# Kernel tuning notes

Measured on AMD Instinct MI355X. Metric: run time of the kernel, lower is better.

Reference implementation:

```python
import jax, jax.numpy as jnp
import numpy as np

HID = 2048
NH = 16
HD = HID // NH  # 128
SEQ = 2048
BSZ = 2
NEG = -1e9


def setup_inputs() -> dict:
    key = jax.random.key(0)
    ks = jax.random.split(key, 9)
    s = 0.02
    hidden_states = jax.random.normal(ks[0], (BSZ, SEQ, HID), jnp.float32)
    # additive causal mask [1,1,S,S]
    causal = jnp.tril(jnp.ones((SEQ, SEQ), jnp.bool_))
    attention_mask = jnp.where(causal, 0.0, NEG).astype(jnp.float32)[None, None]
    Wq = jax.random.normal(ks[1], (HID, NH * HD), jnp.float32) * s
    bq = jax.random.normal(ks[2], (NH * HD,), jnp.float32) * s
    Wk = jax.random.normal(ks[3], (HID, NH * HD), jnp.float32) * s
    bk = jax.random.normal(ks[4], (NH * HD,), jnp.float32) * s
    Wv = jax.random.normal(ks[5], (HID, NH * HD), jnp.float32) * s
    bv = jax.random.normal(ks[6], (NH * HD,), jnp.float32) * s
    Wo = jax.random.normal(ks[7], (NH * HD, HID), jnp.float32) * s
    return {"hidden_states": hidden_states, "attention_mask": attention_mask,
            "Wq": Wq, "bq": bq, "Wk": Wk, "bk": bk, "Wv": Wv, "bv": bv, "Wo": Wo}


def reference(hidden_states, attention_mask, Wq, bq, Wk, bk, Wv, bv, Wo):
    b, s, _ = hidden_states.shape
    # projections -> [b, h, s, d]
    q = (hidden_states @ Wq + bq).reshape(b, s, NH, HD).transpose(0, 2, 1, 3)
    k = (hidden_states @ Wk + bk).reshape(b, s, NH, HD).transpose(0, 2, 1, 3)
    v = (hidden_states @ Wv + bv).reshape(b, s, NH, HD).transpose(0, 2, 1, 3)
    # eager attention, materializing [b,h,s,s] scores as in the original
    scores = jnp.einsum('bhqd,bhkd->bhqk', q, k) / jnp.sqrt(jnp.float32(HD))
    scores = scores + attention_mask
    probs = jax.nn.softmax(scores.astype(jnp.float32), axis=-1).astype(q.dtype)
    ctx = jnp.einsum('bhqk,bhkd->bhqd', probs, v)
    ctx = ctx.transpose(0, 2, 1, 3).reshape(b, s, NH * HD)
    return ctx @ Wo
```

## Files before the change

### kernel.cpp

```cpp
#include <hip/hip_runtime.h>

#define SEQ 2048
#define HIDDEN 2048
#define NHEAD 16
#define HDIM 128
#define BSZ 2

typedef __attribute__((ext_vector_type(8))) short bf16x8;
typedef __attribute__((ext_vector_type(4))) float f32x4;
typedef __attribute__((ext_vector_type(16))) float f32x16;
typedef unsigned short u16;
typedef unsigned int u32;

__device__ __forceinline__ u16 f2bf(float f) {
  union { float f; u32 u; } v; v.f = f;
  u32 r = v.u + 0x7FFF + ((v.u >> 16) & 1);
  return (u16)(r >> 16);
}

__device__ __forceinline__ void gload_lds16(const void* g, void* l) {
  __builtin_amdgcn_global_load_lds((const __attribute__((address_space(1))) u32*)g,
                                   (__attribute__((address_space(3))) u32*)l, 16, 0, 0);
}

__device__ __forceinline__ u32 pkbf(float lo, float hi_) {
  u32 r;
  asm("v_cvt_pk_bf16_f32 %0, %1, %2" : "=v"(r) : "v"(lo), "v"(hi_));
  return r;
}

__device__ __forceinline__ void pl32swap(u32& a, u32& b) {
  asm("v_permlane32_swap_b32 %0, %1" : "+v"(a), "+v"(b));
}

__global__ void conv_hs_kernel(const float4* __restrict__ in, uint4* __restrict__ out) {
  int i = blockIdx.x * 256 + threadIdx.x;
  float4 a = in[2 * i], b = in[2 * i + 1];
  uint4 o;
  o.x = (u32)f2bf(a.x) | ((u32)f2bf(a.y) << 16);
  o.y = (u32)f2bf(a.z) | ((u32)f2bf(a.w) << 16);
  o.z = (u32)f2bf(b.x) | ((u32)f2bf(b.y) << 16);
  o.w = (u32)f2bf(b.z) | ((u32)f2bf(b.w) << 16);
  out[i] = o;
}

__global__ void transw_kernel(const float* __restrict__ W0, const float* __restrict__ W1,
                              const float* __restrict__ W2, const float* __restrict__ W3,
                              u16* __restrict__ T0, u16* __restrict__ T1,
                              u16* __restrict__ T2, u16* __restrict__ T3) {
  __shared__ float tile[32][33];
  const float* W; u16* T;
  switch (blockIdx.z) {
    case 0: W = W0; T = T0; break;
    case 1: W = W1; T = T1; break;
    case 2: W = W2; T = T2; break;
    default: W = W3; T = T3; break;
  }
  int n0 = blockIdx.x * 32, k0 = blockIdx.y * 32;
  int tx = threadIdx.x, ty = threadIdx.y;
  #pragma unroll
  for (int r = ty; r < 32; r += 8) tile[r][tx] = W[(k0 + r) * HIDDEN + n0 + tx];
  __syncthreads();
  #pragma unroll
  for (int r = ty; r < 32; r += 8) T[(n0 + r) * HIDDEN + k0 + tx] = f2bf(tile[tx][r]);
}

__global__ __launch_bounds__(256, 2)
void qkv_gemm(const u16* __restrict__ hsb,
              const u16* __restrict__ wqT, const u16* __restrict__ wkT, const u16* __restrict__ wvT,
              const float* __restrict__ bq, const float* __restrict__ bk, const float* __restrict__ bv,
              u16* __restrict__ Qb, u16* __restrict__ Kb, u16* __restrict__ Vb) {
  __shared__ u16 As[128 * 32];
  __shared__ u16 Bs[128 * 32];
  const int z = blockIdx.z;
  const u16* Bt = (z == 0) ? wqT : (z == 1) ? wkT : wvT;
  const float* bias = (z == 0) ? bq : (z == 1) ? bk : bv;
  u16* dst = (z == 0) ? Qb : (z == 1) ? Kb : Vb;
  const float scale = (z == 0) ? 0.08838834764831845f * 1.4426950408889634f : 1.0f;
  const int m0 = blockIdx.y * 128, n0 = blockIdx.x * 128;
  const int tid = threadIdx.x, lane = tid & 63, w = tid >> 6;
  const int wr = w >> 1, wc = w & 1, l15 = lane & 15, l4 = lane >> 4;

  f32x4 acc[4][4] = {};
  for (int k0 = 0; k0 < HIDDEN; k0 += 32) {
    __syncthreads();
    #pragma unroll
    for (int i = 0; i < 2; i++) {
      int c = tid + i * 256;
      gload_lds16(hsb + (m0 + (c >> 2)) * HIDDEN + k0 + (c & 3) * 8, &As[c * 8]);
    }
    #pragma unroll
    for (int i = 0; i < 2; i++) {
      int c = tid + i * 256;
      gload_lds16(Bt + (n0 + (c >> 2)) * HIDDEN + k0 + (c & 3) * 8, &Bs[c * 8]);
    }
    __syncthreads();
    bf16x8 a[4], b[4];
    #pragma unroll
    for (int mi = 0; mi < 4; mi++)
      a[mi] = *(const bf16x8*)&As[(wr * 64 + mi * 16 + l15) * 32 + l4 * 8];
    #pragma unroll
    for (int ni = 0; ni < 4; ni++)
      b[ni] = *(const bf16x8*)&Bs[(wc * 64 + ni * 16 + l15) * 32 + l4 * 8];
    #pragma unroll
    for (int mi = 0; mi < 4; mi++)
      #pragma unroll
      for (int ni = 0; ni < 4; ni++)
        acc[mi][ni] = __builtin_amdgcn_mfma_f32_16x16x32_bf16(a[mi], b[ni], acc[mi][ni], 0, 0, 0);
  }
  #pragma unroll
  for (int mi = 0; mi < 4; mi++) {
    #pragma unroll
    for (int ni = 0; ni < 4; ni++) {
      int n = n0 + wc * 64 + ni * 16 + l15;
      float bv_ = bias[n];
      int h_ = n >> 7, d_ = n & 127;
      #pragma unroll
      for (int r = 0; r < 4; r++) {
        int m = m0 + wr * 64 + mi * 16 + l4 * 4 + r;
        int b_ = m >> 11, s_ = m & 2047;
        dst[(((b_ * NHEAD + h_) * SEQ) + s_) * HDIM + d_] = f2bf((acc[mi][ni][r] + bv_) * scale);
      }
    }
  }
}

__global__ void transv_kernel(const u16* __restrict__ V, u16* __restrict__ VT) {
  __shared__ u16 tile[32][33];
  int bh = blockIdx.z;
  int d0 = blockIdx.x * 32, s0 = blockIdx.y * 32;
  const u16* Vp = V + (size_t)bh * SEQ * HDIM;
  u16* Tp = VT + (size_t)bh * HDIM * SEQ;
  int tx = threadIdx.x, ty = threadIdx.y;
  #pragma unroll
  for (int r = ty; r < 32; r += 8) tile[r][tx] = Vp[(s0 + r) * HDIM + d0 + tx];
  __syncthreads();
  #pragma unroll
  for (int r = ty; r < 32; r += 8) Tp[(d0 + r) * SEQ + s0 + tx] = tile[tx][r];
}

__device__ __forceinline__ void stage_tiles(u16* KLb, u16* VLb,
                                            const u16* Kg0, const u16* Vg0,
                                            int j, int w, int lane) {
  const u16* Kg = Kg0 + j * (64 * HDIM);
  const u16* Vg = Vg0 + j * 64;
  #pragma unroll
  for (int i = 0; i < 4; i++) {
    const int c = (w * 4 + i) * 64 + lane;
    const int row = c >> 4;
    const int inb = ((c & 15) * 16) ^ ((row & 7) << 4);
    gload_lds16(Kg + row * HDIM + (inb >> 1), (char*)KLb + c * 16);
  }
  #pragma unroll
  for (int i = 0; i < 4; i++) {
    const int c = (w * 4 + i) * 64 + lane;
    const int row = c >> 3;
    const int inb = ((c & 7) * 16) ^ ((row & 7) << 4);
    gload_lds16(Vg + row * SEQ + (inb >> 1), (char*)VLb + c * 16);
  }
}

__global__ __launch_bounds__(256)
void attn_kernel(const u16* __restrict__ Qb, const u16* __restrict__ Kb,
                 const u16* __restrict__ VbT, u16* __restrict__ ctx) {
  __shared__ u16 KL[2][64 * 128];
  __shared__ u16 VL[2][128 * 64];

  const int n = blockIdx.x;
  const int xcd = n & 7, slot = n >> 3;
  const int bh = xcd * 4 + (slot >> 3);
  const int xp = slot & 7;
  const int b = bh >> 4, h = bh & 15;
  const int tid = threadIdx.x, lane = tid & 63, w = tid >> 6;
  const int l31 = lane & 31, hi = lane >> 5;

  const u16* Kg0 = Kb + (size_t)bh * SEQ * HDIM;
  const u16* Vg0 = VbT + (size_t)bh * HDIM * SEQ;
  const u16* Qg0 = Qb + (size_t)bh * SEQ * HDIM;

  for (int ph = 0; ph < 2; ph++) {
    const int qt = ph ? (15 - xp) : xp;
    const int NT = 2 * qt + 2;
    const int q0w = qt * 128 + w * 32;
    const int qlane = q0w + l31;

    bf16x8 qf[8];
    #pragma unroll
    for (int c = 0; c < 8; c++)
      qf[c] = *(const bf16x8*)(Qg0 + (size_t)qlane * HDIM + c * 16 + hi * 8);

    f32x16 o0 = {}, o1 = {}, o2 = {}, o3 = {};
    float m_run = -1e30f, l_run = 0.0f;

    int cb = 0;
    stage_tiles(&KL[0][0], &VL[0][0], Kg0, Vg0, 0, w, lane);
    __syncthreads();

    for (int j = 0; j < NT; j++) {
      if (j + 1 < NT)
        stage_tiles(&KL[cb ^ 1][0], &VL[cb ^ 1][0], Kg0, Vg0, j + 1, w, lane);

      f32x16 s0 = {}, s1 = {};
      #pragma unroll
      for (int c = 0; c < 8; c++) {
        const int cbyte = c * 32 + hi * 16;
        const int r0 = l31, r1 = 32 + l31;
        bf16x8 k0 = *(const bf16x8*)((const char*)&KL[cb][0] + (r0 * 256 + (cbyte ^ ((r0 & 7) << 4))));
        bf16x8 k1 = *(const bf16x8*)((const char*)&KL[cb][0] + (r1 * 256 + (cbyte ^ ((r1 & 7) << 4))));
        s0 = __builtin_amdgcn_mfma_f32_32x32x16_bf16(k0, qf[c], s0, 0, 0, 0);
        s1 = __builtin_amdgcn_mfma_f32_32x32x16_bf16(k1, qf[c], s1, 0, 0, 0);
      }

      if (j >= NT - 2) {
        const int kvb = j * 64 + 4 * hi;
        #pragma unroll
        for (int r = 0; r < 16; r++) {
          const int kr = kvb + (r & 3) + 8 * (r >> 2);
          if (kr > qlane) s0[r] = -1e9f;
          if (kr + 32 > qlane) s1[r] = -1e9f;
        }
      }

      float pm = s0[0];
      #pragma unroll
      for (int r = 1; r < 16; r++) pm = fmaxf(pm, s0[r]);
      #pragma unroll
      for (int r = 0; r < 16; r++) pm = fmaxf(pm, s1[r]);
      pm = fmaxf(pm, __shfl_xor(pm, 32));

      if (!__all(pm - m_run <= 8.0f)) {
        const float mn = fmaxf(m_run, pm);
        const float al = exp2f(m_run - mn);
        l_run *= al;
        #pragma unroll
        for (int r = 0; r < 16; r++) {
          const float ar = __shfl(al, (r & 3) + 8 * (r >> 2) + 4 * hi);
          o0[r] *= ar; o1[r] *= ar; o2[r] *= ar; o3[r] *= ar;
        }
        m_run = mn;
      }

      float rs = 0.0f;
      #pragma unroll
      for (int r = 0; r < 16; r++) { s0[r] = exp2f(s0[r] - m_run); rs += s0[r]; }
      #pragma unroll
      for (int r = 0; r < 16; r++) { s1[r] = exp2f(s1[r] - m_run); rs += s1[r]; }
      rs += __shfl_xor(rs, 32);
      l_run += rs;

      union { u32 wd[4]; bf16x8 v; } pa0, pa1, pa2, pa3;
      { u32 A0 = pkbf(s0[0], s0[1]),  B0 = pkbf(s0[4], s0[5]);  pl32swap(A0, B0);
        u32 A1 = pkbf(s0[2], s0[3]),  B1 = pkbf(s0[6], s0[7]);  pl32swap(A1, B1);
        pa0.wd[0] = A0; pa0.wd[1] = A1; pa0.wd[2] = B0; pa0.wd[3] = B1; }
      { u32 A0 = pkbf(s0[8], s0[9]),  B0 = pkbf(s0[12], s0[13]); pl32swap(A0, B0);
        u32 A1 = pkbf(s0[10], s0[11]), B1 = pkbf(s0[14], s0[15]); pl32swap(A1, B1);
        pa1.wd[0] = A0; pa1.wd[1] = A1; pa1.wd[2] = B0; pa1.wd[3] = B1; }
      { u32 A0 = pkbf(s1[0], s1[1]),  B0 = pkbf(s1[4], s1[5]);  pl32swap(A0, B0);
        u32 A1 = pkbf(s1[2], s1[3]),  B1 = pkbf(s1[6], s1[7]);  pl32swap(A1, B1);
        pa2.wd[0] = A0; pa2.wd[1] = A1; pa2.wd[2] = B0; pa2.wd[3] = B1; }
      { u32 A0 = pkbf(s1[8], s1[9]),  B0 = pkbf(s1[12], s1[13]); pl32swap(A0, B0);
        u32 A1 = pkbf(s1[10], s1[11]), B1 = pkbf(s1[14], s1[15]); pl32swap(A1, B1);
        pa3.wd[0] = A0; pa3.wd[1] = A1; pa3.wd[2] = B0; pa3.wd[3] = B1; }

#define PV_D(OD, DS) { \
      const int row = (DS) * 32 + l31; \
      const int sw = (row & 7) << 4; \
      const char* vbase = (const char*)&VL[cb][0] + row * 128; \
      bf16x8 v0 = *(const bf16x8*)(vbase + ((  0 + hi * 16) ^ sw)); \
      bf16x8 v1 = *(const bf16x8*)(vbase + (( 32 + hi * 16) ^ sw)); \
      bf16x8 v2 = *(const bf16x8*)(vbase + (( 64 + hi * 16) ^ sw)); \
      bf16x8 v3 = *(const bf16x8*)(vbase + (( 96 + hi * 16) ^ sw)); \
      OD = __builtin_amdgcn_mfma_f32_32x32x16_bf16(pa0.v, v0, OD, 0, 0, 0); \
      OD = __builtin_amdgcn_mfma_f32_32x32x16_bf16(pa1.v, v1, OD, 0, 0, 0); \
      OD = __builtin_amdgcn_mfma_f32_32x32x16_bf16(pa2.v, v2, OD, 0, 0, 0); \
      OD = __builtin_amdgcn_mfma_f32_32x32x16_bf16(pa3.v, v3, OD, 0, 0, 0); }
      PV_D(o0, 0) PV_D(o1, 1) PV_D(o2, 2) PV_D(o3, 3)
#undef PV_D

      __syncthreads();
      cb ^= 1;
    }

    const float invl = 1.0f / l_run;
    #pragma unroll
    for (int r = 0; r < 16; r++) {
      const int qr = (r & 3) + 8 * (r >> 2) + 4 * hi;
      const float iv = __shfl(invl, qr);
      const size_t base = ((size_t)b * SEQ + (q0w + qr)) * HIDDEN + h * HDIM + l31;
      ctx[base +  0] = f2bf(o0[r] * iv);
      ctx[base + 32] = f2bf(o1[r] * iv);
      ctx[base + 64] = f2bf(o2[r] * iv);
      ctx[base + 96] = f2bf(o3[r] * iv);
    }
  }
}

__global__ __launch_bounds__(256, 2)
void out_gemm(const u16* __restrict__ ctxb, const u16* __restrict__ woT, float* __restrict__ out) {
  __shared__ u16 As[128 * 32];
  __shared__ u16 Bs[128 * 32];
  const int m0 = blockIdx.y * 128, n0 = blockIdx.x * 128;
  const int tid = threadIdx.x, lane = tid & 63, w = tid >> 6;
  const int wr = w >> 1, wc = w & 1, l15 = lane & 15, l4 = lane >> 4;

  f32x4 acc[4][4] = {};
  for (int k0 = 0; k0 < HIDDEN; k0 += 32) {
    __syncthreads();
    #pragma unroll
    for (int i = 0; i < 2; i++) {
      int c = tid + i * 256;
      gload_lds16(ctxb + (m0 + (c >> 2)) * HIDDEN + k0 + (c & 3) * 8, &As[c * 8]);
    }
    #pragma unroll
    for (int i = 0; i < 2; i++) {
      int c = tid + i * 256;
      gload_lds16(woT + (n0 + (c >> 2)) * HIDDEN + k0 + (c & 3) * 8, &Bs[c * 8]);
    }
    __syncthreads();
    bf16x8 a[4], b[4];
    #pragma unroll
    for (int mi = 0; mi < 4; mi++)
      a[mi] = *(const bf16x8*)&As[(wr * 64 + mi * 16 + l15) * 32 + l4 * 8];
    #pragma unroll
    for (int ni = 0; ni < 4; ni++)
      b[ni] = *(const bf16x8*)&Bs[(wc * 64 + ni * 16 + l15) * 32 + l4 * 8];
    #pragma unroll
    for (int mi = 0; mi < 4; mi++)
      #pragma unroll
      for (int ni = 0; ni < 4; ni++)
        acc[mi][ni] = __builtin_amdgcn_mfma_f32_16x16x32_bf16(a[mi], b[ni], acc[mi][ni], 0, 0, 0);
  }
  #pragma unroll
  for (int mi = 0; mi < 4; mi++)
    #pragma unroll
    for (int ni = 0; ni < 4; ni++) {
      int n = n0 + wc * 64 + ni * 16 + l15;
      #pragma unroll
      for (int r = 0; r < 4; r++) {
        int m = m0 + wr * 64 + mi * 16 + l4 * 4 + r;
        out[(size_t)m * HIDDEN + n] = acc[mi][ni][r];
      }
    }
}

extern "C" void kernel_launch(void* const* d_in, const int* in_sizes, int n_in,
                              void* d_out, int out_size, void* d_ws, size_t ws_size,
                              hipStream_t stream) {
  const float* hs = (const float*)d_in[0];
  const float* Wq = (const float*)d_in[2];
  const float* bq = (const float*)d_in[3];
  const float* Wk = (const float*)d_in[4];
  const float* bk = (const float*)d_in[5];
  const float* Wv = (const float*)d_in[6];
  const float* bv = (const float*)d_in[7];
  const float* Wo = (const float*)d_in[8];
  float* out = (float*)d_out;

  char* ws = (char*)d_ws;
  const size_t MB = 1024 * 1024;
  u16* hsb = (u16*)(ws + 0);
  u16* wqT = (u16*)(ws + 16 * MB);
  u16* wkT = (u16*)(ws + 24 * MB);
  u16* wvT = (u16*)(ws + 32 * MB);
  u16* woT = (u16*)(ws + 40 * MB);
  u16* Qb  = (u16*)(ws + 48 * MB);
  u16* Kb  = (u16*)(ws + 64 * MB);
  u16* Vb  = (u16*)(ws + 80 * MB);
  u16* VbT = (u16*)(ws + 0);
  u16* ctx = (u16*)(ws + 16 * MB);

  conv_hs_kernel<<<4096, 256, 0, stream>>>((const float4*)hs, (uint4*)hsb);
  transw_kernel<<<dim3(64, 64, 4), dim3(32, 8), 0, stream>>>(Wq, Wk, Wv, Wo, wqT, wkT, wvT, woT);
  qkv_gemm<<<dim3(16, 32, 3), 256, 0, stream>>>(hsb, wqT, wkT, wvT, bq, bk, bv, Qb, Kb, Vb);
  transv_kernel<<<dim3(4, 64, 32), dim3(32, 8), 0, stream>>>(Vb, VbT);
  attn_kernel<<<dim3(256), 256, 0, stream>>>(Qb, Kb, VbT, ctx);
  out_gemm<<<dim3(16, 32, 1), 256, 0, stream>>>(ctx, woT, out);
  (void)in_sizes; (void)n_in; (void)out_size; (void)ws_size;
}
```

Baseline: 430.4 us.

## Replace QKV and output GEMMs with pipelined 256x128 swizzled-LDS 8-wave kernel

Rewrites both projection GEMMs around a shared 512-thread core with 128x256 tiles, a 64-wide K step, XOR-swizzled LDS and double-buffered async global-to-LDS staging interleaved with MFMA phases. The QKV GEMM treats the three transposed weight matrices as one contiguous N=6144 operand, and block indices are remapped for cache locality. The goal is to hide global load latency and avoid LDS bank conflicts that the old synchronous 128x128 loop exposed. It relies on the workspace layout keeping wqT, wkT and wvT adjacent, and on hand-tuned vmcnt wait counts.

```diff
diff --git a/kernel.cpp b/kernel.cpp
--- a/kernel.cpp
+++ b/kernel.cpp
@@ -65,64 +65,144 @@
   for (int r = ty; r < 32; r += 8) T[(n0 + r) * HIDDEN + k0 + tx] = f2bf(tile[tx][r]);
 }
 
-__global__ __launch_bounds__(256, 2)
-void qkv_gemm(const u16* __restrict__ hsb,
-              const u16* __restrict__ wqT, const u16* __restrict__ wkT, const u16* __restrict__ wvT,
-              const float* __restrict__ bq, const float* __restrict__ bk, const float* __restrict__ bv,
-              u16* __restrict__ Qb, u16* __restrict__ Kb, u16* __restrict__ Vb) {
-  __shared__ u16 As[128 * 32];
-  __shared__ u16 Bs[128 * 32];
-  const int z = blockIdx.z;
-  const u16* Bt = (z == 0) ? wqT : (z == 1) ? wkT : wvT;
+__device__ __forceinline__ void stageA8(const u16* Ag, u16* Al, int kt, int h, int tid) {
+  const int c = tid;
+  const int row = h * 64 + (c >> 3);
+  const int slot = (c & 7) ^ (row & 7);
+  gload_lds16(Ag + (size_t)row * HIDDEN + kt * 64 + slot * 8,
+              (char*)Al + h * 8192 + c * 16);
+}
+__device__ __forceinline__ void stageB8(const u16* Bg, u16* Bl, int kt, int h, int tid) {
+  #pragma unroll
+  for (int i = 0; i < 2; i++) {
+    const int c = tid + i * 512;
+    const int row = h * 128 + (c >> 3);
+    const int slot = (c & 7) ^ (row & 7);
+    gload_lds16(Bg + (size_t)row * HIDDEN + kt * 64 + slot * 8,
+                (char*)Bl + h * 16384 + c * 16);
+  }
+}
+
+#define LDA8(dst, QA, mi, ks) { \
+  const int row_ = (QA) * 64 + wr * 32 + (mi) * 16 + l15; \
+  dst = *(const bf16x8*)((const char*)Acur + row_ * 128 + ((((ks) * 4 + l4) ^ (row_ & 7)) * 16)); }
+#define LDB8(dst, QB, ni, ks) { \
+  const int row_ = (QB) * 128 + wc * 32 + (ni) * 16 + l15; \
+  dst = *(const bf16x8*)((const char*)Bcur + row_ * 128 + ((((ks) * 4 + l4) ^ (row_ & 7)) * 16)); }
+
+#define MFMA_(a, b, c) __builtin_amdgcn_mfma_f32_16x16x32_bf16(a, b, c, 0, 0, 0)
+
+#define PHASE8(QA, QB, STG, VM) { \
+  bf16x8 a00, a10, a01, a11, b00, b10, b01, b11; \
+  LDA8(a00, QA, 0, 0) LDA8(a10, QA, 1, 0) LDA8(a01, QA, 0, 1) LDA8(a11, QA, 1, 1) \
+  LDB8(b00, QB, 0, 0) LDB8(b10, QB, 1, 0) LDB8(b01, QB, 0, 1) LDB8(b11, QB, 1, 1) \
+  STG; \
+  __builtin_amdgcn_s_barrier(); \
+  __builtin_amdgcn_s_setprio(1); \
+  acc[QA][QB][0][0] = MFMA_(a00, b00, acc[QA][QB][0][0]); \
+  acc[QA][QB][0][1] = MFMA_(a00, b10, acc[QA][QB][0][1]); \
+  acc[QA][QB][1][0] = MFMA_(a10, b00, acc[QA][QB][1][0]); \
+  acc[QA][QB][1][1] = MFMA_(a10, b10, acc[QA][QB][1][1]); \
+  acc[QA][QB][0][0] = MFMA_(a01, b01, acc[QA][QB][0][0]); \
+  acc[QA][QB][0][1] = MFMA_(a01, b11, acc[QA][QB][0][1]); \
+  acc[QA][QB][1][0] = MFMA_(a11, b01, acc[QA][QB][1][0]); \
+  acc[QA][QB][1][1] = MFMA_(a11, b11, acc[QA][QB][1][1]); \
+  __builtin_amdgcn_s_setprio(0); \
+  asm volatile("s_waitcnt vmcnt(" VM ")" ::: "memory"); \
+  __builtin_amdgcn_sched_barrier(0); \
+  __builtin_amdgcn_s_barrier(); }
+
+#define GEMM8_CORE(Ag, Bg) \
+  __shared__ u16 AL[2][128 * 64]; \
+  __shared__ u16 BL[2][256 * 64]; \
+  const int tid = threadIdx.x, lane = tid & 63, w = tid >> 6; \
+  const int wr = w >> 2, wc = w & 3, l15 = lane & 15, l4 = (lane >> 4) & 3; \
+  f32x4 acc[2][2][2][2] = {}; \
+  stageA8(Ag, AL[0], 0, 0, tid); \
+  __builtin_amdgcn_sched_barrier(0); \
+  stageB8(Bg, BL[0], 0, 0, tid); \
+  __builtin_amdgcn_sched_barrier(0); \
+  stageB8(Bg, BL[0], 0, 1, tid); \
+  __builtin_amdgcn_sched_barrier(0); \
+  stageA8(Ag, AL[0], 0, 1, tid); \
+  asm volatile("s_waitcnt vmcnt(3)" ::: "memory"); \
+  __builtin_amdgcn_sched_barrier(0); \
+  __builtin_amdgcn_s_barrier(); \
+  for (int t = 0; t < HIDDEN / 64; t++) { \
+    const int cb = t & 1; \
+    const u16* Acur = AL[cb]; const u16* Bcur = BL[cb]; \
+    u16* An = AL[cb ^ 1]; u16* Bn = BL[cb ^ 1]; \
+    const int kn = (t < HIDDEN / 64 - 1) ? t + 1 : t;   \
+    PHASE8(0, 0, stageA8(Ag, An, kn, 0, tid), "2") \
+    PHASE8(0, 1, stageB8(Bg, Bn, kn, 0, tid), "3") \
+    PHASE8(1, 0, stageB8(Bg, Bn, kn, 1, tid), "5") \
+    PHASE8(1, 1, stageA8(Ag, An, kn, 1, tid), "3") \
+  }
+
+__global__ __launch_bounds__(512, 1)
+void qkv_gemm8(const u16* __restrict__ hsb, const u16* __restrict__ wT,
+               const float* __restrict__ bq, const float* __restrict__ bk,
+               const float* __restrict__ bv,
+               u16* __restrict__ Qb, u16* __restrict__ Kb, u16* __restrict__ Vb) {
+  const int o = blockIdx.x;
+  const int wg = (o & 7) * 96 + (o >> 3);
+  const int by = wg / 24, bx = wg % 24;
+  const int z = bx >> 3;
+  const u16* Ag = hsb + (size_t)by * 128 * HIDDEN;
+  const u16* Bg = wT + (size_t)bx * 256 * HIDDEN;
+  u16* dst = (z == 0) ? Qb : (z == 1) ? Kb : Vb;
   const float* bias = (z == 0) ? bq : (z == 1) ? bk : bv;
-  u16* dst = (z == 0) ? Qb : (z == 1) ? Kb : Vb;
   const float scale = (z == 0) ? 0.08838834764831845f * 1.4426950408889634f : 1.0f;
-  const int m0 = blockIdx.y * 128, n0 = blockIdx.x * 128;
-  const int tid = threadIdx.x, lane = tid & 63, w = tid >> 6;
-  const int wr = w >> 1, wc = w & 1, l15 = lane & 15, l4 = lane >> 4;
-
-  f32x4 acc[4][4] = {};
-  for (int k0 = 0; k0 < HIDDEN; k0 += 32) {
-    __syncthreads();
+
+  GEMM8_CORE(Ag, Bg)
+
+  #pragma unroll
+  for (int qa = 0; qa < 2; qa++)
     #pragma unroll
-    for (int i = 0; i < 2; i++) {
-      int c = tid + i * 256;
-      gload_lds16(hsb + (m0 + (c >> 2)) * HIDDEN + k0 + (c & 3) * 8, &As[c * 8]);
-    }
+    for (int qb = 0; qb < 2; qb++)
+      #pragma unroll
+      for (int ni = 0; ni < 2; ni++) {
+        const int n = bx * 256 + qb * 128 + wc * 32 + ni * 16 + l15;
+        const int h_ = (n >> 7) & 15, d_ = n & 127;
+        const float bv_ = bias[n & 2047];
+        #pragma unroll
+        for (int mi = 0; mi < 2; mi++)
+          #pragma unroll
+          for (int r = 0; r < 4; r++) {
+            const int m = by * 128 + qa * 64 + wr * 32 + mi * 16 + l4 * 4 + r;
+            const int b_ = m >> 11, s_ = m & 2047;
+            dst[(((size_t)(b_ * NHEAD + h_) * SEQ) + s_) * HDIM + d_] =
+                f2bf((acc[qa][qb][mi][ni][r] + bv_) * scale);
+          }
+      }
+}
+
+__global__ __launch_bounds__(512, 1)
+void out_gemm8(const u16* __restrict__ ctxb, const u16* __restrict__ woT,
+               float* __restrict__ out) {
+  const int o = blockIdx.x;
+  const int wg = (o & 7) * 32 + (o >> 3);
+  const int by = wg >> 3, bx = wg & 7;
+  const u16* Ag = ctxb + (size_t)by * 128 * HIDDEN;
+  const u16* Bg = woT + (size_t)bx * 256 * HIDDEN;
+
+  GEMM8_CORE(Ag, Bg)
+
+  #pragma unroll
+  for (int qa = 0; qa < 2; qa++)
     #pragma unroll
-    for (int i = 0; i < 2; i++) {
-      int c = tid + i * 256;
-      gload_lds16(Bt + (n0 + (c >> 2)) * HIDDEN + k0 + (c & 3) * 8, &Bs[c * 8]);
-    }
-    __syncthreads();
-    bf16x8 a[4], b[4];
-    #pragma unroll
-    for (int mi = 0; mi < 4; mi++)
-      a[mi] = *(const bf16x8*)&As[(wr * 64 + mi * 16 + l15) * 32 + l4 * 8];
-    #pragma unroll
-    for (int ni = 0; ni < 4; ni++)
-      b[ni] = *(const bf16x8*)&Bs[(wc * 64 + ni * 16 + l15) * 32 + l4 * 8];
-    #pragma unroll
-    for (int mi = 0; mi < 4; mi++)
-      #pragma unroll
-      for (int ni = 0; ni < 4; ni++)
-        acc[mi][ni] = __builtin_amdgcn_mfma_f32_16x16x32_bf16(a[mi], b[ni], acc[mi][ni], 0, 0, 0);
-  }
-  #pragma unroll
-  for (int mi = 0; mi < 4; mi++) {
-    #pragma unroll
-    for (int ni = 0; ni < 4; ni++) {
-      int n = n0 + wc * 64 + ni * 16 + l15;
-      float bv_ = bias[n];
-      int h_ = n >> 7, d_ = n & 127;
-      #pragma unroll
-      for (int r = 0; r < 4; r++) {
-        int m = m0 + wr * 64 + mi * 16 + l4 * 4 + r;
-        int b_ = m >> 11, s_ = m & 2047;
-        dst[(((b_ * NHEAD + h_) * SEQ) + s_) * HDIM + d_] = f2bf((acc[mi][ni][r] + bv_) * scale);
+    for (int qb = 0; qb < 2; qb++)
+      #pragma unroll
+      for (int ni = 0; ni < 2; ni++) {
+        const int n = bx * 256 + qb * 128 + wc * 32 + ni * 16 + l15;
+        #pragma unroll
+        for (int mi = 0; mi < 2; mi++)
+          #pragma unroll
+          for (int r = 0; r < 4; r++) {
+            const int m = by * 128 + qa * 64 + wr * 32 + mi * 16 + l4 * 4 + r;
+            out[(size_t)m * HIDDEN + n] = acc[qa][qb][mi][ni][r];
+          }
       }
-    }
-  }
 }
 
 __global__ void transv_kernel(const u16* __restrict__ V, u16* __restrict__ VT) {
@@ -295,54 +375,6 @@
   }
 }
 
-__global__ __launch_bounds__(256, 2)
-void out_gemm(const u16* __restrict__ ctxb, const u16* __restrict__ woT, float* __restrict__ out) {
-  __shared__ u16 As[128 * 32];
-  __shared__ u16 Bs[128 * 32];
-  const int m0 = blockIdx.y * 128, n0 = blockIdx.x * 128;
-  const int tid = threadIdx.x, lane = tid & 63, w = tid >> 6;
-  const int wr = w >> 1, wc = w & 1, l15 = lane & 15, l4 = lane >> 4;
-
-  f32x4 acc[4][4] = {};
-  for (int k0 = 0; k0 < HIDDEN; k0 += 32) {
-    __syncthreads();
-    #pragma unroll
-    for (int i = 0; i < 2; i++) {
-      int c = tid + i * 256;
-      gload_lds16(ctxb + (m0 + (c >> 2)) * HIDDEN + k0 + (c & 3) * 8, &As[c * 8]);
-    }
-    #pragma unroll
-    for (int i = 0; i < 2; i++) {
-      int c = tid + i * 256;
-      gload_lds16(woT + (n0 + (c >> 2)) * HIDDEN + k0 + (c & 3) * 8, &Bs[c * 8]);
-    }
-    __syncthreads();
-    bf16x8 a[4], b[4];
-    #pragma unroll
-    for (int mi = 0; mi < 4; mi++)
-      a[mi] = *(const bf16x8*)&As[(wr * 64 + mi * 16 + l15) * 32 + l4 * 8];
-    #pragma unroll
-    for (int ni = 0; ni < 4; ni++)
-      b[ni] = *(const bf16x8*)&Bs[(wc * 64 + ni * 16 + l15) * 32 + l4 * 8];
-    #pragma unroll
-    for (int mi = 0; mi < 4; mi++)
-      #pragma unroll
-      for (int ni = 0; ni < 4; ni++)
-        acc[mi][ni] = __builtin_amdgcn_mfma_f32_16x16x32_bf16(a[mi], b[ni], acc[mi][ni], 0, 0, 0);
-  }
-  #pragma unroll
-  for (int mi = 0; mi < 4; mi++)
-    #pragma unroll
-    for (int ni = 0; ni < 4; ni++) {
-      int n = n0 + wc * 64 + ni * 16 + l15;
-      #pragma unroll
-      for (int r = 0; r < 4; r++) {
-        int m = m0 + wr * 64 + mi * 16 + l4 * 4 + r;
-        out[(size_t)m * HIDDEN + n] = acc[mi][ni][r];
-      }
-    }
-}
-
 extern "C" void kernel_launch(void* const* d_in, const int* in_sizes, int n_in,
                               void* d_out, int out_size, void* d_ws, size_t ws_size,
                               hipStream_t stream) {
@@ -371,9 +403,9 @@
 
   conv_hs_kernel<<<4096, 256, 0, stream>>>((const float4*)hs, (uint4*)hsb);
   transw_kernel<<<dim3(64, 64, 4), dim3(32, 8), 0, stream>>>(Wq, Wk, Wv, Wo, wqT, wkT, wvT, woT);
-  qkv_gemm<<<dim3(16, 32, 3), 256, 0, stream>>>(hsb, wqT, wkT, wvT, bq, bk, bv, Qb, Kb, Vb);
+  qkv_gemm8<<<768, 512, 0, stream>>>(hsb, wqT, bq, bk, bv, Qb, Kb, Vb);
   transv_kernel<<<dim3(4, 64, 32), dim3(32, 8), 0, stream>>>(Vb, VbT);
   attn_kernel<<<dim3(256), 256, 0, stream>>>(Qb, Kb, VbT, ctx);
-  out_gemm<<<dim3(16, 32, 1), 256, 0, stream>>>(ctx, woT, out);
+  out_gemm8<<<256, 512, 0, stream>>>(ctx, woT, out);
   (void)in_sizes; (void)n_in; (void)out_size; (void)ws_size;
 }
```

Result: slower. 471.3 us (+9.5%).
